# Kernel tuning notes

Measured on AMD Instinct MI355X. Metric: run time of the kernel, lower is better.

Reference implementation:

```python
import jax, jax.numpy as jnp
import numpy as np

NEG_SLOPE = 0.2  # PyG GATConv default negative_slope
EPS = 1e-16      # PyG softmax denominator epsilon


def gat_conv(x, src, dst, W, b, att_src, att_dst, num_nodes):
    """PyG GATConv, heads=1, add_self_loops=True (self loops already in src/dst).
    x: [N, Fin]; src/dst: [E]; W: [Fin, Fout]; att_src/att_dst: [Fout]."""
    h = x @ W                                  # [N, Fout]
    a_src = h @ att_src                        # [N]
    a_dst = h @ att_dst                        # [N]
    e = jax.nn.leaky_relu(a_src[src] + a_dst[dst], NEG_SLOPE)  # [E]
    m = jax.ops.segment_max(e, dst, num_segments=num_nodes)    # softmax over edges grouped by dst
    ex = jnp.exp(e - m[dst])
    denom = jax.ops.segment_sum(ex, dst, num_segments=num_nodes)
    alpha = ex / (denom[dst] + EPS)            # [E]
    out = jax.ops.segment_sum(alpha[:, None] * h[src], dst, num_segments=num_nodes)
    return out + b


def global_attention(x, gate_w, gate_b):
    """PyG GlobalAttention with a single graph: softmax(gate_nn(x)) weighted sum."""
    gate = x @ gate_w + gate_b                 # [N, 1]
    attn = jax.nn.softmax(gate, axis=0)        # softmax over all nodes (one graph)
    return jnp.sum(attn * x, axis=0, keepdims=True)  # [1, F]


def setup_inputs() -> dict:
    key = jax.random.key(0)
    ks = jax.random.split(key, 12)
    N, E, D, H = 50000, 800000, 768, 256
    x = jax.random.normal(ks[0], (N, D), dtype=jnp.float32)
    edge_index = jax.random.randint(ks[1], (2, E), 0, N, dtype=jnp.int64)
    s = 1.0 / np.sqrt(D)
    W1 = jax.random.normal(ks[2], (D, H), dtype=jnp.float32) * s
    b1 = jnp.zeros((H,), dtype=jnp.float32)
    as1 = jax.random.normal(ks[3], (H,), dtype=jnp.float32) * (1.0 / np.sqrt(H))
    ad1 = jax.random.normal(ks[4], (H,), dtype=jnp.float32) * (1.0 / np.sqrt(H))
    s2 = 1.0 / np.sqrt(H)
    W2 = jax.random.normal(ks[5], (H, H), dtype=jnp.float32) * s2
    b2 = jnp.zeros((H,), dtype=jnp.float32)
    as2 = jax.random.normal(ks[6], (H,), dtype=jnp.float32) * s2
    ad2 = jax.random.normal(ks[7], (H,), dtype=jnp.float32) * s2
    gate_w = jax.random.normal(ks[8], (H, 1), dtype=jnp.float32) * s2
    gate_b = jnp.zeros((1,), dtype=jnp.float32)
    return {"x": x, "edge_index": edge_index, "W1": W1, "b1": b1, "as1": as1,
            "ad1": ad1, "W2": W2, "b2": b2, "as2": as2, "ad2": ad2,
            "gate_w": gate_w, "gate_b": gate_b}


def reference(x, edge_index, W1, b1, as1, ad1, W2, b2, as2, ad2, gate_w, gate_b):
    N = x.shape[0]
    loops = jnp.arange(N, dtype=edge_index.dtype)
    src = jnp.concatenate([edge_index[0], loops])  # add self loops (GATConv default)
    dst = jnp.concatenate([edge_index[1], loops])
    h = gat_conv(x, src, dst, W1, b1, as1, ad1, N)
    h = jax.nn.relu(h)
    h = gat_conv(h, src, dst, W2, b2, as2, ad2, N)
    h = jax.nn.relu(h)
    return global_attention(h, gate_w, gate_b)   # [1, 256]
```

## Files before the change

### kernel.cpp

```cpp
#include <hip/hip_runtime.h>

#define WAVE 64
#define LRELU(x) ((x) > 0.0f ? (x) : 0.2f * (x))

typedef __attribute__((ext_vector_type(8))) short bf16x8;
typedef __attribute__((ext_vector_type(8))) unsigned short u16x8;
typedef __attribute__((ext_vector_type(4))) float f32x4;

__device__ __forceinline__ void gld16(const void* g, void* l) {
    __builtin_amdgcn_global_load_lds((const __attribute__((address_space(1))) unsigned int*)g,
                                     (__attribute__((address_space(3))) unsigned int*)l,
                                     16, 0, 0);
}

__device__ __forceinline__ unsigned short f2bf_hi(float f) {
    unsigned u = __builtin_bit_cast(unsigned, f);
    u += 0x7FFF + ((u >> 16) & 1);
    return (unsigned short)(u >> 16);
}

__device__ __forceinline__ void split8(f32x4 a, f32x4 b, bf16x8& hi, bf16x8& lo) {
    float f[8] = {a[0], a[1], a[2], a[3], b[0], b[1], b[2], b[3]};
#pragma unroll
    for (int e = 0; e < 8; e++) {
        unsigned u = __builtin_bit_cast(unsigned, f[e]);
        float hf = __builtin_bit_cast(float, u & 0xFFFF0000u);
        float fl = f[e] - hf;
        unsigned u2 = __builtin_bit_cast(unsigned, fl);
        unsigned t2 = u2 + 0x7FFF + ((u2 >> 16) & 1);
        hi[e] = (short)(u >> 16);
        lo[e] = (short)(t2 >> 16);
    }
}

__global__ __launch_bounds__(256) void k_gemm_f32A(const float* __restrict__ A,
                                                   const unsigned short* __restrict__ Bh,
                                                   unsigned short* __restrict__ Cb,
                                                   float* __restrict__ asrc,
                                                   float* __restrict__ adst,
                                                   const float* __restrict__ att_s,
                                                   const float* __restrict__ att_d,
                                                   int M, int K) {
    __shared__ char smem[24576];
    char* SAH = smem;
    char* SAL = smem + 8192;
    char* SBH = smem + 16384;

    const int tid = threadIdx.x, lane = tid & 63, w = tid >> 6;
    const int m16 = lane & 15, q = lane >> 4;
    const int row0 = blockIdx.x * 128, col0 = blockIdx.y * 128;

    f32x4 acc[4][4];
#pragma unroll
    for (int i = 0; i < 4; i++)
#pragma unroll
        for (int j = 0; j < 4; j++) acc[i][j] = (f32x4){0.f, 0.f, 0.f, 0.f};

    const int s_row = tid >> 1;
    const int s_mt  = s_row >> 4, s_m16 = s_row & 15;
    const int s_q0  = (tid & 1) * 2;
    int s_grow = row0 + s_row;
    if (s_grow > M - 1) s_grow = M - 1;
    const f32x4* aptr = (const f32x4*)&A[(size_t)s_grow * K] + (tid & 1) * 4;
    const int s_off = (s_mt * 4 + s_q0) * 256 + s_m16 * 16;

    const int b_rloc = lane >> 2;
    const int b_kb   = (lane & 3) * 16;

    f32x4 pre0 = aptr[0], pre1 = aptr[1], pre2 = aptr[2], pre3 = aptr[3];

    for (int k0 = 0; k0 < K; k0 += 32) {
#pragma unroll
        for (int s = 0; s < 2; s++) {
            int c = w * 2 + s;
            int brow = col0 + c * 16 + b_rloc;
            gld16((const char*)Bh + ((size_t)brow * K + k0) * 2 + b_kb, SBH + c * 1024);
        }
        {
            bf16x8 h0, l0, h1, l1;
            split8(pre0, pre1, h0, l0);
            split8(pre2, pre3, h1, l1);
            *(bf16x8*)(SAH + s_off)       = h0;
            *(bf16x8*)(SAL + s_off)       = l0;
            *(bf16x8*)(SAH + s_off + 256) = h1;
            *(bf16x8*)(SAL + s_off + 256) = l1;
        }
        __syncthreads();

        if (k0 + 32 < K) {
            aptr += 8;
            pre0 = aptr[0]; pre1 = aptr[1]; pre2 = aptr[2]; pre3 = aptr[3];
        }

        bf16x8 bh[4];
#pragma unroll
        for (int nt = 0; nt < 4; nt++) {
            int r = (w & 1) * 64 + nt * 16 + m16;
            bh[nt] = *(bf16x8*)(SBH + r * 64 + q * 16);
        }
#pragma unroll
        for (int mt = 0; mt < 4; mt++) {
            int frag = ((w >> 1) * 4 + mt) * 4 + q;
            bf16x8 ah = *(bf16x8*)(SAH + frag * 256 + m16 * 16);
            bf16x8 al = *(bf16x8*)(SAL + frag * 256 + m16 * 16);
#pragma unroll
            for (int nt = 0; nt < 4; nt++) {
                acc[mt][nt] = __builtin_amdgcn_mfma_f32_16x16x32_bf16(ah, bh[nt], acc[mt][nt], 0, 0, 0);
                acc[mt][nt] = __builtin_amdgcn_mfma_f32_16x16x32_bf16(al, bh[nt], acc[mt][nt], 0, 0, 0);
            }
        }
        __syncthreads();
    }

    const int rbase = row0 + (w >> 1) * 64;
    const int cbase = col0 + (w & 1) * 64;
#pragma unroll
    for (int mt = 0; mt < 4; mt++)
#pragma unroll
        for (int r = 0; r < 4; r++) {
            int row = rbase + mt * 16 + q * 4 + r;
            if (row < M) {
#pragma unroll
                for (int nt = 0; nt < 4; nt++)
                    Cb[(size_t)row * 256 + cbase + nt * 16 + m16] = f2bf_hi(acc[mt][nt][r]);
            }
        }
    float as_v[4], ad_v[4];
#pragma unroll
    for (int nt = 0; nt < 4; nt++) {
        as_v[nt] = att_s[cbase + nt * 16 + m16];
        ad_v[nt] = att_d[cbase + nt * 16 + m16];
    }
#pragma unroll
    for (int mt = 0; mt < 4; mt++)
#pragma unroll
        for (int r = 0; r < 4; r++) {
            float s = 0.f, d = 0.f;
#pragma unroll
            for (int nt = 0; nt < 4; nt++) {
                float v = acc[mt][nt][r];
                s = fmaf(v, as_v[nt], s);
                d = fmaf(v, ad_v[nt], d);
            }
#pragma unroll
            for (int off = 1; off < 16; off <<= 1) {
                s += __shfl_xor(s, off);
                d += __shfl_xor(d, off);
            }
            int row = rbase + mt * 16 + q * 4 + r;
            if (m16 == 0 && row < M) {
                atomicAdd(&asrc[row], s);
                atomicAdd(&adst[row], d);
            }
        }
}

__global__ __launch_bounds__(256) void k_gemm_bf16A(const unsigned short* __restrict__ Ah,
                                                    const unsigned short* __restrict__ Al,
                                                    const unsigned short* __restrict__ Bh,
                                                    unsigned short* __restrict__ Cb,
                                                    float* __restrict__ asrc,
                                                    float* __restrict__ adst,
                                                    const float* __restrict__ att_s,
                                                    const float* __restrict__ att_d,
                                                    int M, int K) {
    __shared__ char smem[24576];
    char* SAH = smem;
    char* SAL = smem + 8192;
    char* SBH = smem + 16384;

    const int tid = threadIdx.x, lane = tid & 63, w = tid >> 6;
    const int m16 = lane & 15, q = lane >> 4;
    const int row0 = blockIdx.x * 128, col0 = blockIdx.y * 128;

    f32x4 acc[4][4];
#pragma unroll
    for (int i = 0; i < 4; i++)
#pragma unroll
        for (int j = 0; j < 4; j++) acc[i][j] = (f32x4){0.f, 0.f, 0.f, 0.f};

    const int rloc = lane >> 2;
    const int kb   = (lane & 3) * 16;

    for (int k0 = 0; k0 < K; k0 += 32) {
#pragma unroll
        for (int s = 0; s < 2; s++) {
            int c = w * 2 + s;
            int arow = row0 + c * 16 + rloc;
            int brow = col0 + c * 16 + rloc;
            gld16((const char*)Ah + ((size_t)arow * K + k0) * 2 + kb, SAH + c * 1024);
            gld16((const char*)Al + ((size_t)arow * K + k0) * 2 + kb, SAL + c * 1024);
            gld16((const char*)Bh + ((size_t)brow * K + k0) * 2 + kb, SBH + c * 1024);
        }
        __syncthreads();

        bf16x8 bh[4];
#pragma unroll
        for (int nt = 0; nt < 4; nt++) {
            int r = (w & 1) * 64 + nt * 16 + m16;
            bh[nt] = *(bf16x8*)(SBH + r * 64 + q * 16);
        }
#pragma unroll
        for (int mt = 0; mt < 4; mt++) {
            int r = (w >> 1) * 64 + mt * 16 + m16;
            bf16x8 ah = *(bf16x8*)(SAH + r * 64 + q * 16);
            bf16x8 al = *(bf16x8*)(SAL + r * 64 + q * 16);
#pragma unroll
            for (int nt = 0; nt < 4; nt++) {
                acc[mt][nt] = __builtin_amdgcn_mfma_f32_16x16x32_bf16(ah, bh[nt], acc[mt][nt], 0, 0, 0);
                acc[mt][nt] = __builtin_amdgcn_mfma_f32_16x16x32_bf16(al, bh[nt], acc[mt][nt], 0, 0, 0);
            }
        }
        __syncthreads();
    }

    const int rbase = row0 + (w >> 1) * 64;
    const int cbase = col0 + (w & 1) * 64;
#pragma unroll
    for (int mt = 0; mt < 4; mt++)
#pragma unroll
        for (int r = 0; r < 4; r++) {
            int row = rbase + mt * 16 + q * 4 + r;
            if (row < M) {
#pragma unroll
                for (int nt = 0; nt < 4; nt++)
                    Cb[(size_t)row * 256 + cbase + nt * 16 + m16] = f2bf_hi(acc[mt][nt][r]);
            }
        }
    float as_v[4], ad_v[4];
#pragma unroll
    for (int nt = 0; nt < 4; nt++) {
        as_v[nt] = att_s[cbase + nt * 16 + m16];
        ad_v[nt] = att_d[cbase + nt * 16 + m16];
    }
#pragma unroll
    for (int mt = 0; mt < 4; mt++)
#pragma unroll
        for (int r = 0; r < 4; r++) {
            float s = 0.f, d = 0.f;
#pragma unroll
            for (int nt = 0; nt < 4; nt++) {
                float v = acc[mt][nt][r];
                s = fmaf(v, as_v[nt], s);
                d = fmaf(v, ad_v[nt], d);
            }
#pragma unroll
            for (int off = 1; off < 16; off <<= 1) {
                s += __shfl_xor(s, off);
                d += __shfl_xor(d, off);
            }
            int row = rbase + mt * 16 + q * 4 + r;
            if (m16 == 0 && row < M) {
                atomicAdd(&asrc[row], s);
                atomicAdd(&adst[row], d);
            }
        }
}

__global__ __launch_bounds__(256) void k_convB(const float* __restrict__ W,
                                               unsigned short* __restrict__ BThi, int K) {
    int idx = blockIdx.x * 256 + threadIdx.x;
    int k = idx >> 8, n = idx & 255;
    if (k >= K) return;
    BThi[(size_t)n * K + k] = f2bf_hi(W[(size_t)k * 256 + n]);
}

__global__ __launch_bounds__(256) void k_degree(const int* __restrict__ dst,
                                                int* __restrict__ counts, int E) {
    int e = blockIdx.x * 256 + threadIdx.x;
    if (e < E) atomicAdd(&counts[dst[e]], 1);
}

__global__ __launch_bounds__(256) void k_part(const int* __restrict__ counts,
                                              int* __restrict__ psum, int N) {
    __shared__ int red[256];
    int tid = threadIdx.x;
    int i = blockIdx.x * 256 + tid;
    red[tid] = (i < N) ? counts[i] : 0;
    __syncthreads();
    for (int off = 128; off; off >>= 1) {
        if (tid < off) red[tid] += red[tid + off];
        __syncthreads();
    }
    if (tid == 0) psum[blockIdx.x] = red[0];
}

__global__ __launch_bounds__(256) void k_scan_part(int* __restrict__ psum, int nb,
                                                   int* __restrict__ total_out) {
    __shared__ int s[256];
    int tid = threadIdx.x;
    int v = (tid < nb) ? psum[tid] : 0;
    s[tid] = v;
    __syncthreads();
    for (int off = 1; off < 256; off <<= 1) {
        int t = (tid >= off) ? s[tid - off] : 0;
        __syncthreads();
        s[tid] += t;
        __syncthreads();
    }
    if (tid < nb) psum[tid] = s[tid] - v;
    if (tid == 255) *total_out = s[255];
}

__global__ __launch_bounds__(256) void k_rowptr(const int* __restrict__ counts,
                                                const int* __restrict__ psum,
                                                int* __restrict__ rowptr,
                                                int* __restrict__ cursor, int N) {
    __shared__ int s[256];
    int tid = threadIdx.x;
    int i = blockIdx.x * 256 + tid;
    int v = (i < N) ? counts[i] : 0;
    s[tid] = v;
    __syncthreads();
    for (int off = 1; off < 256; off <<= 1) {
        int t = (tid >= off) ? s[tid - off] : 0;
        __syncthreads();
        s[tid] += t;
        __syncthreads();
    }
    if (i < N) {
        int excl = psum[blockIdx.x] + s[tid] - v;
        rowptr[i] = excl;
        cursor[i] = excl;
    }
}

__global__ __launch_bounds__(256) void k_scatter(const int* __restrict__ src,
                                                 const int* __restrict__ dst,
                                                 int* __restrict__ cursor,
                                                 int* __restrict__ col, int E) {
    int e = blockIdx.x * 256 + threadIdx.x;
    if (e < E) {
        int p = atomicAdd(&cursor[dst[e]], 1);
        col[p] = src[e];
    }
}

__global__ __launch_bounds__(256) void k_edge(const unsigned short* __restrict__ hb,
                                              const float* __restrict__ asrc,
                                              const float* __restrict__ adst,
                                              const float* __restrict__ gmaxv,
                                              const int* __restrict__ rowptr,
                                              const int* __restrict__ col,
                                              const float* __restrict__ bias,
                                              float* __restrict__ outf,
                                              unsigned short* __restrict__ outh,
                                              unsigned short* __restrict__ outl,
                                              const float* __restrict__ gw,
                                              const float* __restrict__ gb,
                                              float* __restrict__ gatep, int N) {
    int hw = threadIdx.x >> 5;
    int l  = threadIdx.x & 31;
    int node = blockIdx.x * 8 + hw;
    if (node >= N) return;
    int j = rowptr[node], end = rowptr[node + 1];
    float ad = adst[node];
    float m = LRELU(gmaxv[0] + ad);

    float a[8];
    float wself = __expf(LRELU(asrc[node] + ad) - m);
    u16x8 hv = *(const u16x8*)&hb[(size_t)node * 256 + l * 8];
#pragma unroll
    for (int e = 0; e < 8; e++)
        a[e] = wself * __builtin_bit_cast(float, (unsigned)hv[e] << 16);
    float denom = wself;

    for (; j + 4 <= end; j += 4) {
        int s0 = col[j], s1 = col[j + 1], s2 = col[j + 2], s3 = col[j + 3];
        float w0 = __expf(LRELU(asrc[s0] + ad) - m);
        float w1 = __expf(LRELU(asrc[s1] + ad) - m);
        float w2 = __expf(LRELU(asrc[s2] + ad) - m);
        float w3 = __expf(LRELU(asrc[s3] + ad) - m);
        denom += w0 + w1 + w2 + w3;
        u16x8 h0 = *(const u16x8*)&hb[(size_t)s0 * 256 + l * 8];
        u16x8 h1 = *(const u16x8*)&hb[(size_t)s1 * 256 + l * 8];
        u16x8 h2 = *(const u16x8*)&hb[(size_t)s2 * 256 + l * 8];
        u16x8 h3 = *(const u16x8*)&hb[(size_t)s3 * 256 + l * 8];
#pragma unroll
        for (int e = 0; e < 8; e++) {
            float f0 = __builtin_bit_cast(float, (unsigned)h0[e] << 16);
            float f1 = __builtin_bit_cast(float, (unsigned)h1[e] << 16);
            float f2 = __builtin_bit_cast(float, (unsigned)h2[e] << 16);
            float f3 = __builtin_bit_cast(float, (unsigned)h3[e] << 16);
            a[e] = fmaf(w0, f0, fmaf(w1, f1, fmaf(w2, f2, fmaf(w3, f3, a[e]))));
        }
    }
    for (; j < end; j++) {
        int s = col[j];
        float wgt = __expf(LRELU(asrc[s] + ad) - m);
        denom += wgt;
        u16x8 hx = *(const u16x8*)&hb[(size_t)s * 256 + l * 8];
#pragma unroll
        for (int e = 0; e < 8; e++)
            a[e] = fmaf(wgt, __builtin_bit_cast(float, (unsigned)hx[e] << 16), a[e]);
    }
    float inv = 1.0f / (denom + 1e-16f);
#pragma unroll
    for (int e = 0; e < 8; e++) a[e] *= inv;

    float o[8];
    {
        float4 bv0 = *(const float4*)&bias[l * 8];
        float4 bv1 = *(const float4*)&bias[l * 8 + 4];
        float bb[8] = {bv0.x, bv0.y, bv0.z, bv0.w, bv1.x, bv1.y, bv1.z, bv1.w};
#pragma unroll
        for (int e = 0; e < 8; e++) o[e] = fmaxf(a[e] + bb[e], 0.0f);
    }
    if (outf) {
        float4 o0 = make_float4(o[0], o[1], o[2], o[3]);
        float4 o1 = make_float4(o[4], o[5], o[6], o[7]);
        *(float4*)&outf[(size_t)node * 256 + l * 8]     = o0;
        *(float4*)&outf[(size_t)node * 256 + l * 8 + 4] = o1;
    }
    if (outh) {
        u16x8 ph, pl;
#pragma unroll
        for (int e = 0; e < 8; e++) {
            unsigned u = __builtin_bit_cast(unsigned, o[e]);
            float hf = __builtin_bit_cast(float, u & 0xFFFF0000u);
            float fl = o[e] - hf;
            unsigned u2 = __builtin_bit_cast(unsigned, fl);
            unsigned t2 = u2 + 0x7FFF + ((u2 >> 16) & 1);
            ph[e] = (unsigned short)(u >> 16);
            pl[e] = (unsigned short)(t2 >> 16);
        }
        *(u16x8*)&outh[(size_t)node * 256 + l * 8] = ph;
        *(u16x8*)&outl[(size_t)node * 256 + l * 8] = pl;
    }
    if (gatep) {
        float s = 0.f;
#pragma unroll
        for (int e = 0; e < 8; e++) s = fmaf(o[e], gw[l * 8 + e], s);
#pragma unroll
        for (int off = 16; off; off >>= 1) s += __shfl_xor(s, off);
        if (l == 0) gatep[node] = s + gb[0];
    }
}

__global__ __launch_bounds__(256) void k_pmax(const float* __restrict__ v, int N,
                                              float* __restrict__ pmax) {
    __shared__ float red[256];
    int tid = threadIdx.x;
    float m = -3.0e38f;
    for (int i = blockIdx.x * 256 + tid; i < N; i += gridDim.x * 256) m = fmaxf(m, v[i]);
    red[tid] = m;
    __syncthreads();
    for (int off = 128; off; off >>= 1) {
        if (tid < off) red[tid] = fmaxf(red[tid], red[tid + off]);
        __syncthreads();
    }
    if (tid == 0) pmax[blockIdx.x] = red[0];
}

__global__ __launch_bounds__(64) void k_fold(const float* __restrict__ p,
                                             float* __restrict__ o) {
    int lane = threadIdx.x;
    float m = p[lane];
#pragma unroll
    for (int off = 32; off; off >>= 1) m = fmaxf(m, __shfl_xor(m, off));
    if (lane == 0) o[0] = m;
}

__global__ __launch_bounds__(256) void k_gmid(const float* __restrict__ pmax, int nb,
                                              float* __restrict__ scal,
                                              float* __restrict__ gout) {
    __shared__ float red[256];
    int tid = threadIdx.x;
    red[tid] = (tid < nb) ? pmax[tid] : -3.0e38f;
    __syncthreads();
    for (int off = 128; off; off >>= 1) {
        if (tid < off) red[tid] = fmaxf(red[tid], red[tid + off]);
        __syncthreads();
    }
    if (tid == 0) { scal[0] = red[0]; scal[1] = 0.0f; }
    gout[tid] = 0.0f;
}

__global__ __launch_bounds__(256) void k_gout(const float* __restrict__ h,
                                              const float* __restrict__ gate,
                                              float* __restrict__ scal_rw,
                                              float* __restrict__ gout, int N) {
    int f = threadIdx.x;
    float gmax = scal_rw[0];
    float acc = 0.0f, sumw = 0.0f;
    for (int i = blockIdx.x; i < N; i += gridDim.x) {
        float w = __expf(gate[i] - gmax);
        acc = fmaf(w, h[(size_t)i * 256 + f], acc);
        sumw += w;
    }
    atomicAdd(&gout[f], acc);
    if (f == 0) atomicAdd(&scal_rw[1], sumw);
}

__global__ __launch_bounds__(256) void k_final(const float* __restrict__ gout,
                                               const float* __restrict__ scal,
                                               float* __restrict__ out) {
    int f = threadIdx.x;
    out[f] = gout[f] / scal[1];
}

extern "C" void kernel_launch(void* const* d_in, const int* in_sizes, int n_in,
                              void* d_out, int out_size, void* d_ws, size_t ws_size,
                              hipStream_t stream) {
    const float* x   = (const float*)d_in[0];
    const int*   ei  = (const int*)d_in[1];
    const float* W1  = (const float*)d_in[2];
    const float* b1  = (const float*)d_in[3];
    const float* as1 = (const float*)d_in[4];
    const float* ad1 = (const float*)d_in[5];
    const float* W2  = (const float*)d_in[6];
    const float* b2  = (const float*)d_in[7];
    const float* as2 = (const float*)d_in[8];
    const float* ad2 = (const float*)d_in[9];
    const float* gw  = (const float*)d_in[10];
    const float* gb  = (const float*)d_in[11];
    float* out = (float*)d_out;

    const int N = in_sizes[0] / 768;
    const int E = in_sizes[1] / 2;
    const int Mpad = (N + 127) & ~127;
    const int* srcA = ei;
    const int* dstA = ei + E;

    char* w = (char*)d_ws;
    auto alloc = [&](size_t bytes) -> void* {
        void* p = (void*)w;
        w += (bytes + 255) & ~(size_t)255;
        return p;
    };
    unsigned short* bufHb = (unsigned short*)alloc((size_t)N * 256 * 2);
    unsigned short* X2h = (unsigned short*)alloc((size_t)Mpad * 256 * 2);
    unsigned short* X2l = (unsigned short*)alloc((size_t)Mpad * 256 * 2);
    float* bufX = (float*)X2h;
    float* asrc   = (float*)alloc((size_t)N * 4);
    float* adst   = (float*)alloc((size_t)N * 4);
    float* gate   = (float*)alloc((size_t)N * 4);
    int*   counts = (int*)alloc((size_t)N * 4);
    int*   rowptr = (int*)alloc((size_t)(N + 1) * 4);
    int*   cursor = (int*)alloc((size_t)N * 4);
    int*   colbuf = (int*)alloc((size_t)E * 4);
    int*   psum   = (int*)alloc(256 * 4);
    float* pmax   = (float*)alloc(256 * 4);
    float* gmaxv  = (float*)alloc(4 * 4);
    float* scal   = (float*)alloc(8 * 4);
    float* gout   = (float*)alloc(256 * 4);
    unsigned short* BT1 = (unsigned short*)alloc((size_t)256 * 768 * 2);
    unsigned short* BT2 = (unsigned short*)alloc((size_t)256 * 256 * 2);

    const int eb  = (E + 255) / 256;
    const int nb8 = (N + 7) / 8;
    const int nb  = (N + 255) / 256;
    const dim3 gg(Mpad / 128, 2);

    k_convB<<<768, 256, 0, stream>>>(W1, BT1, 768);
    k_convB<<<256, 256, 0, stream>>>(W2, BT2, 256);

    (void)hipMemsetAsync(counts, 0, (size_t)N * 4, stream);
    k_degree<<<eb, 256, 0, stream>>>(dstA, counts, E);
    k_part<<<nb, 256, 0, stream>>>(counts, psum, N);
    k_scan_part<<<1, 256, 0, stream>>>(psum, nb, rowptr + N);
    k_rowptr<<<nb, 256, 0, stream>>>(counts, psum, rowptr, cursor, N);
    k_scatter<<<eb, 256, 0, stream>>>(srcA, dstA, cursor, colbuf, E);

    (void)hipMemsetAsync(asrc, 0, (size_t)N * 4, stream);
    (void)hipMemsetAsync(adst, 0, (size_t)N * 4, stream);
    k_gemm_f32A<<<gg, 256, 0, stream>>>(x, BT1, bufHb, asrc, adst, as1, ad1, N, 768);
    k_pmax<<<64, 256, 0, stream>>>(asrc, N, pmax);
    k_fold<<<1, 64, 0, stream>>>(pmax, gmaxv);
    k_edge<<<nb8, 256, 0, stream>>>(bufHb, asrc, adst, gmaxv, rowptr, colbuf, b1,
                                    nullptr, X2h, X2l, nullptr, nullptr, nullptr, N);

    (void)hipMemsetAsync(asrc, 0, (size_t)N * 4, stream);
    (void)hipMemsetAsync(adst, 0, (size_t)N * 4, stream);
    k_gemm_bf16A<<<gg, 256, 0, stream>>>(X2h, X2l, BT2, bufHb, asrc, adst, as2, ad2, N, 256);
    k_pmax<<<64, 256, 0, stream>>>(asrc, N, pmax);
    k_fold<<<1, 64, 0, stream>>>(pmax, gmaxv);
    k_edge<<<nb8, 256, 0, stream>>>(bufHb, asrc, adst, gmaxv, rowptr, colbuf, b2,
                                    bufX, nullptr, nullptr, gw, gb, gate, N);

    k_pmax<<<64, 256, 0, stream>>>(gate, N, pmax);
    k_gmid<<<1, 256, 0, stream>>>(pmax, 64, scal, gout);
    k_gout<<<256, 256, 0, stream>>>(bufX, gate, scal, gout, N);
    k_final<<<1, 256, 0, stream>>>(gout, scal, out);
}
```

Measured before the change: 614.2 us.

## Multi-buffer GEMM operand staging with async LDS loads and manual waitcnt pipelining

Both GEMM kernels now stage A in a triple-buffered and B in a double-buffered LDS layout, loaded with direct global-to-LDS loads issued one to two k-tiles ahead. Explicit vmcnt waits and raw barriers replace __syncthreads so that loads overlap the MFMA work. The fp32-A kernel now loads raw fp32 into LDS and does the hi/lo bf16 split after reading from LDS, with the low part truncated instead of rounded. This is meant to hide global load latency, at the cost of 64KB of LDS per block (lower occupancy) and a slightly different precision in the low-part split.

```diff
diff --git a/kernel.cpp b/kernel.cpp
--- a/kernel.cpp
+++ b/kernel.cpp
@@ -2,6 +2,7 @@
 
 #define WAVE 64
 #define LRELU(x) ((x) > 0.0f ? (x) : 0.2f * (x))
+#define SB0 __builtin_amdgcn_sched_barrier(0)
 
 typedef __attribute__((ext_vector_type(8))) short bf16x8;
 typedef __attribute__((ext_vector_type(8))) unsigned short u16x8;
@@ -33,6 +34,19 @@
     }
 }
 
+__device__ __forceinline__ void split8t(f32x4 a, f32x4 b, bf16x8& hi, bf16x8& lo) {
+    float f[8] = {a[0], a[1], a[2], a[3], b[0], b[1], b[2], b[3]};
+#pragma unroll
+    for (int e = 0; e < 8; e++) {
+        unsigned u = __builtin_bit_cast(unsigned, f[e]);
+        float hf = __builtin_bit_cast(float, u & 0xFFFF0000u);
+        float fl = f[e] - hf;
+        unsigned u2 = __builtin_bit_cast(unsigned, fl);
+        hi[e] = (short)(u >> 16);
+        lo[e] = (short)(u2 >> 16);
+    }
+}
+
 __global__ __launch_bounds__(256) void k_gemm_f32A(const float* __restrict__ A,
                                                    const unsigned short* __restrict__ Bh,
                                                    unsigned short* __restrict__ Cb,
@@ -41,14 +55,14 @@
                                                    const float* __restrict__ att_s,
                                                    const float* __restrict__ att_d,
                                                    int M, int K) {
-    __shared__ char smem[24576];
-    char* SAH = smem;
-    char* SAL = smem + 8192;
-    char* SBH = smem + 16384;
+    __shared__ char smem[65536];
+    char* bA = smem;
+    char* bB = smem + 49152;
 
     const int tid = threadIdx.x, lane = tid & 63, w = tid >> 6;
     const int m16 = lane & 15, q = lane >> 4;
     const int row0 = blockIdx.x * 128, col0 = blockIdx.y * 128;
+    const int NT = K >> 5;
 
     f32x4 acc[4][4];
 #pragma unroll
@@ -56,60 +70,71 @@
 #pragma unroll
         for (int j = 0; j < 4; j++) acc[i][j] = (f32x4){0.f, 0.f, 0.f, 0.f};
 
-    const int s_row = tid >> 1;
-    const int s_mt  = s_row >> 4, s_m16 = s_row & 15;
-    const int s_q0  = (tid & 1) * 2;
-    int s_grow = row0 + s_row;
-    if (s_grow > M - 1) s_grow = M - 1;
-    const f32x4* aptr = (const f32x4*)&A[(size_t)s_grow * K] + (tid & 1) * 4;
-    const int s_off = (s_mt * 4 + s_q0) * 256 + s_m16 * 16;
-
-    const int b_rloc = lane >> 2;
-    const int b_kb   = (lane & 3) * 16;
-
-    f32x4 pre0 = aptr[0], pre1 = aptr[1], pre2 = aptr[2], pre3 = aptr[3];
-
-    for (int k0 = 0; k0 < K; k0 += 32) {
-#pragma unroll
-        for (int s = 0; s < 2; s++) {
-            int c = w * 2 + s;
-            int brow = col0 + c * 16 + b_rloc;
-            gld16((const char*)Bh + ((size_t)brow * K + k0) * 2 + b_kb, SBH + c * 1024);
-        }
-        {
-            bf16x8 h0, l0, h1, l1;
-            split8(pre0, pre1, h0, l0);
-            split8(pre2, pre3, h1, l1);
-            *(bf16x8*)(SAH + s_off)       = h0;
-            *(bf16x8*)(SAL + s_off)       = l0;
-            *(bf16x8*)(SAH + s_off + 256) = h1;
-            *(bf16x8*)(SAL + s_off + 256) = l1;
-        }
-        __syncthreads();
-
-        if (k0 + 32 < K) {
-            aptr += 8;
-            pre0 = aptr[0]; pre1 = aptr[1]; pre2 = aptr[2]; pre3 = aptr[3];
-        }
-
+    const float* apt[4];
+    const int jA0 = w * 4;
+#pragma unroll
+    for (int jj = 0; jj < 4; jj++) {
+        int j = jA0 + jj;
+        int r = row0 + (j & 1) * 64 + lane;
+        if (r > M - 1) r = M - 1;
+        apt[jj] = A + (size_t)r * K + (j >> 1) * 4;
+    }
+    const unsigned short* bpt[2];
+    const int jB0 = w * 2;
+#pragma unroll
+    for (int jj = 0; jj < 2; jj++) {
+        int j = jB0 + jj;
+        bpt[jj] = Bh + (size_t)(col0 + (j & 1) * 64 + lane) * K + (j >> 1) * 8;
+    }
+
+    auto stageA = [&](int t, int buf) {
+#pragma unroll
+        for (int jj = 0; jj < 4; jj++)
+            gld16(apt[jj] + (size_t)t * 32, bA + buf * 16384 + (jA0 + jj) * 1024);
+    };
+    auto stageB = [&](int t, int buf) {
+#pragma unroll
+        for (int jj = 0; jj < 2; jj++)
+            gld16(bpt[jj] + (size_t)t * 32, bB + buf * 8192 + (jB0 + jj) * 1024);
+    };
+
+    stageB(0, 0); SB0;
+    stageA(0, 0); SB0;
+    stageA(1, 1); SB0;
+    asm volatile("s_waitcnt vmcnt(4)" ::: "memory");
+    __builtin_amdgcn_s_barrier();
+
+    for (int t = 0; t < NT; ++t) {
+        if (t + 1 < NT) stageB(t + 1, (t + 1) & 1);
+        SB0;
+        if (t + 2 < NT) stageA(t + 2, (t + 2) % 3);
+        SB0;
+
+        const char* A_ = bA + (t % 3) * 16384;
+        const char* B_ = bB + (t & 1) * 8192;
         bf16x8 bh[4];
 #pragma unroll
         for (int nt = 0; nt < 4; nt++) {
             int r = (w & 1) * 64 + nt * 16 + m16;
-            bh[nt] = *(bf16x8*)(SBH + r * 64 + q * 16);
+            bh[nt] = *(const bf16x8*)(B_ + q * 2048 + r * 16);
         }
 #pragma unroll
         for (int mt = 0; mt < 4; mt++) {
-            int frag = ((w >> 1) * 4 + mt) * 4 + q;
-            bf16x8 ah = *(bf16x8*)(SAH + frag * 256 + m16 * 16);
-            bf16x8 al = *(bf16x8*)(SAL + frag * 256 + m16 * 16);
+            int r = (w >> 1) * 64 + mt * 16 + m16;
+            f32x4 a0 = *(const f32x4*)(A_ + (2 * q) * 2048 + r * 16);
+            f32x4 a1 = *(const f32x4*)(A_ + (2 * q + 1) * 2048 + r * 16);
+            bf16x8 ah, al;
+            split8t(a0, a1, ah, al);
 #pragma unroll
             for (int nt = 0; nt < 4; nt++) {
                 acc[mt][nt] = __builtin_amdgcn_mfma_f32_16x16x32_bf16(ah, bh[nt], acc[mt][nt], 0, 0, 0);
                 acc[mt][nt] = __builtin_amdgcn_mfma_f32_16x16x32_bf16(al, bh[nt], acc[mt][nt], 0, 0, 0);
             }
         }
-        __syncthreads();
+        SB0;
+        if (t + 2 < NT) asm volatile("s_waitcnt vmcnt(4)" ::: "memory");
+        else            asm volatile("s_waitcnt vmcnt(0)" ::: "memory");
+        __builtin_amdgcn_s_barrier();
     }
 
     const int rbase = row0 + (w >> 1) * 64;
@@ -164,14 +189,15 @@
                                                     const float* __restrict__ att_s,
                                                     const float* __restrict__ att_d,
                                                     int M, int K) {
-    __shared__ char smem[24576];
-    char* SAH = smem;
-    char* SAL = smem + 8192;
-    char* SBH = smem + 16384;
+    __shared__ char smem[65536];
+    char* bAh = smem;
+    char* bAl = smem + 24576;
+    char* bB  = smem + 49152;
 
     const int tid = threadIdx.x, lane = tid & 63, w = tid >> 6;
     const int m16 = lane & 15, q = lane >> 4;
     const int row0 = blockIdx.x * 128, col0 = blockIdx.y * 128;
+    const int NT = K >> 5;
 
     f32x4 acc[4][4];
 #pragma unroll
@@ -179,39 +205,70 @@
 #pragma unroll
         for (int j = 0; j < 4; j++) acc[i][j] = (f32x4){0.f, 0.f, 0.f, 0.f};
 
-    const int rloc = lane >> 2;
-    const int kb   = (lane & 3) * 16;
-
-    for (int k0 = 0; k0 < K; k0 += 32) {
-#pragma unroll
-        for (int s = 0; s < 2; s++) {
-            int c = w * 2 + s;
-            int arow = row0 + c * 16 + rloc;
-            int brow = col0 + c * 16 + rloc;
-            gld16((const char*)Ah + ((size_t)arow * K + k0) * 2 + kb, SAH + c * 1024);
-            gld16((const char*)Al + ((size_t)arow * K + k0) * 2 + kb, SAL + c * 1024);
-            gld16((const char*)Bh + ((size_t)brow * K + k0) * 2 + kb, SBH + c * 1024);
-        }
-        __syncthreads();
-
+    const unsigned short* ahpt[2];
+    const unsigned short* alpt[2];
+    const unsigned short* bpt[2];
+    const int j0 = w * 2;
+#pragma unroll
+    for (int jj = 0; jj < 2; jj++) {
+        int j = j0 + jj;
+        int ar = row0 + (j & 1) * 64 + lane;
+        int br = col0 + (j & 1) * 64 + lane;
+        ahpt[jj] = Ah + (size_t)ar * K + (j >> 1) * 8;
+        alpt[jj] = Al + (size_t)ar * K + (j >> 1) * 8;
+        bpt[jj]  = Bh + (size_t)br * K + (j >> 1) * 8;
+    }
+
+    auto stageA = [&](int t, int buf) {
+#pragma unroll
+        for (int jj = 0; jj < 2; jj++)
+            gld16(ahpt[jj] + (size_t)t * 32, bAh + buf * 8192 + (j0 + jj) * 1024);
+#pragma unroll
+        for (int jj = 0; jj < 2; jj++)
+            gld16(alpt[jj] + (size_t)t * 32, bAl + buf * 8192 + (j0 + jj) * 1024);
+    };
+    auto stageB = [&](int t, int buf) {
+#pragma unroll
+        for (int jj = 0; jj < 2; jj++)
+            gld16(bpt[jj] + (size_t)t * 32, bB + buf * 8192 + (j0 + jj) * 1024);
+    };
+
+    stageB(0, 0); SB0;
+    stageA(0, 0); SB0;
+    stageA(1, 1); SB0;
+    asm volatile("s_waitcnt vmcnt(4)" ::: "memory");
+    __builtin_amdgcn_s_barrier();
+
+    for (int t = 0; t < NT; ++t) {
+        if (t + 1 < NT) stageB(t + 1, (t + 1) & 1);
+        SB0;
+        if (t + 2 < NT) stageA(t + 2, (t + 2) % 3);
+        SB0;
+
+        const char* Ah_ = bAh + (t % 3) * 8192;
+        const char* Al_ = bAl + (t % 3) * 8192;
+        const char* B_  = bB  + (t & 1) * 8192;
         bf16x8 bh[4];
 #pragma unroll
         for (int nt = 0; nt < 4; nt++) {
             int r = (w & 1) * 64 + nt * 16 + m16;
-            bh[nt] = *(bf16x8*)(SBH + r * 64 + q * 16);
+            bh[nt] = *(const bf16x8*)(B_ + q * 2048 + r * 16);
         }
 #pragma unroll
         for (int mt = 0; mt < 4; mt++) {
             int r = (w >> 1) * 64 + mt * 16 + m16;
-            bf16x8 ah = *(bf16x8*)(SAH + r * 64 + q * 16);
-            bf16x8 al = *(bf16x8*)(SAL + r * 64 + q * 16);
+            bf16x8 ah = *(const bf16x8*)(Ah_ + q * 2048 + r * 16);
+            bf16x8 al = *(const bf16x8*)(Al_ + q * 2048 + r * 16);
 #pragma unroll
             for (int nt = 0; nt < 4; nt++) {
                 acc[mt][nt] = __builtin_amdgcn_mfma_f32_16x16x32_bf16(ah, bh[nt], acc[mt][nt], 0, 0, 0);
                 acc[mt][nt] = __builtin_amdgcn_mfma_f32_16x16x32_bf16(al, bh[nt], acc[mt][nt], 0, 0, 0);
             }
         }
-        __syncthreads();
+        SB0;
+        if (t + 2 < NT) asm volatile("s_waitcnt vmcnt(4)" ::: "memory");
+        else            asm volatile("s_waitcnt vmcnt(0)" ::: "memory");
+        __builtin_amdgcn_s_barrier();
     }
 
     const int rbase = row0 + (w >> 1) * 64;
```

New measurement: 630.1 us. +2.6%, slower.
